# Kernel tuning notes

Measured on AMD Instinct MI355X. Metric: run time of the kernel, lower is better.

The kernel has to match this reference:

```python
import jax, jax.numpy as jnp
import numpy as np

D_MODEL = 512
NH_ATTN = 8
D_STATE = 64
HEADDIM = 128
D_INNER = 2 * D_MODEL          # 1024
NHEADS = D_INNER // HEADDIM    # 8
CONV_K = 4
CONV_DIM = D_INNER + 2 * D_STATE            # 1152
D_IN_PROJ = 2 * D_INNER + 2 * D_STATE + NHEADS  # 2184
B, S, M = 2, 2048, 1024
EPS = 1e-5


def setup_inputs() -> dict:
    key = jax.random.key(0)
    ks = jax.random.split(key, 10)
    s = 0.02
    return {
        'x': jax.random.normal(ks[0], (B, S, D_MODEL), dtype=jnp.float32),
        'memory': jax.random.normal(ks[1], (B, M, D_MODEL), dtype=jnp.float32),
        'pad_mask': jnp.ones((B, S, 1), dtype=jnp.float32),
        'ln1_g': jnp.ones((D_MODEL,)), 'ln1_b': jnp.zeros((D_MODEL,)),
        'ln2_g': jnp.ones((D_MODEL,)), 'ln2_b': jnp.zeros((D_MODEL,)),
        'W_in': jax.random.normal(ks[2], (D_IN_PROJ, D_MODEL)) * s,
        'conv_w': jax.random.normal(ks[3], (CONV_DIM, 1, CONV_K)) * s,
        'conv_b': jnp.zeros((CONV_DIM,)),
        'dt_bias': jnp.log(jnp.expm1(jax.random.uniform(ks[4], (NHEADS,), minval=0.001, maxval=0.1))),
        'A_log': jnp.log(jnp.arange(1, NHEADS + 1, dtype=jnp.float32)),
        'D_skip': jnp.ones((NHEADS,)),
        'rms_w': jnp.ones((D_INNER,)),
        'W_out': jax.random.normal(ks[5], (D_MODEL, D_INNER)) * s,
        'Wqkv': jax.random.normal(ks[6], (3 * D_MODEL, D_MODEL)) * s,
        'bqkv': jnp.zeros((3 * D_MODEL,)),
        'Wo': jax.random.normal(ks[7], (D_MODEL, D_MODEL)) * s,
        'bo': jnp.zeros((D_MODEL,)),
    }


def _layernorm(x, g, b):
    m = jnp.mean(x, axis=-1, keepdims=True)
    v = jnp.mean((x - m) ** 2, axis=-1, keepdims=True)
    return (x - m) * jax.lax.rsqrt(v + EPS) * g + b


def _mamba(x, W_in, conv_w, conv_b, dt_bias, A_log, D_skip, rms_w, W_out):
    b, s, _ = x.shape
    zxbcdt = x @ W_in.T                                     # [b,s,2184]
    z, xBC, dt = jnp.split(zxbcdt, [D_INNER, D_INNER + CONV_DIM], axis=-1)
    # causal depthwise conv over time on (x, B, C)
    xt = jnp.transpose(xBC, (0, 2, 1))                      # [b,C,s]
    xt = jax.lax.conv_general_dilated(
        xt, conv_w, (1,), [(CONV_K - 1, 0)],
        feature_group_count=CONV_DIM,
        dimension_numbers=('NCH', 'OIH', 'NCH'))
    xBC = jax.nn.silu(jnp.transpose(xt, (0, 2, 1)) + conv_b)
    xs, Bm, Cm = jnp.split(xBC, [D_INNER, D_INNER + D_STATE], axis=-1)
    dt = jax.nn.softplus(dt + dt_bias)                      # [b,s,H]
    A = -jnp.exp(A_log)                                     # [H]
    xh = xs.reshape(b, s, NHEADS, HEADDIM)                  # [b,s,H,P]

    def step(h, inps):
        dt_t, B_t, C_t, x_t = inps                          # [b,H],[b,N],[b,N],[b,H,P]
        decay = jnp.exp(dt_t * A)                           # [b,H]
        h = h * decay[..., None, None] + (dt_t[..., None, None] * x_t[..., None]) * B_t[:, None, None, :]
        y = jnp.einsum('bhpn,bn->bhp', h, C_t)
        return h, y

    h0 = jnp.zeros((b, NHEADS, HEADDIM, D_STATE), dtype=x.dtype)
    _, ys = jax.lax.scan(step, h0, (dt.transpose(1, 0, 2), Bm.transpose(1, 0, 2),
                                    Cm.transpose(1, 0, 2), xh.transpose(1, 0, 2, 3)))
    y = ys.transpose(1, 0, 2, 3) + D_skip[None, None, :, None] * xh
    y = y.reshape(b, s, D_INNER) * jax.nn.silu(z)           # gated
    y = y * jax.lax.rsqrt(jnp.mean(y * y, axis=-1, keepdims=True) + EPS) * rms_w
    return y @ W_out.T


def _cross_attn(q_in, memory, Wqkv, bqkv, Wo, bo):
    b, s, _ = q_in.shape
    m = memory.shape[1]
    dh = D_MODEL // NH_ATTN
    q = (q_in @ Wqkv[:D_MODEL].T + bqkv[:D_MODEL]).reshape(b, s, NH_ATTN, dh)
    k = (memory @ Wqkv[D_MODEL:2 * D_MODEL].T + bqkv[D_MODEL:2 * D_MODEL]).reshape(b, m, NH_ATTN, dh)
    v = (memory @ Wqkv[2 * D_MODEL:].T + bqkv[2 * D_MODEL:]).reshape(b, m, NH_ATTN, dh)
    scores = jnp.einsum('bqhd,bkhd->bhqk', q, k) / jnp.sqrt(jnp.asarray(dh, q.dtype))
    p = jax.nn.softmax(scores, axis=-1)
    out = jnp.einsum('bhqk,bkhd->bqhd', p, v).reshape(b, s, D_MODEL)
    return out @ Wo.T + bo


def reference(x, memory, pad_mask, ln1_g, ln1_b, ln2_g, ln2_b, W_in, conv_w, conv_b,
              dt_bias, A_log, D_skip, rms_w, W_out, Wqkv, bqkv, Wo, bo):
    residual = x
    xn = _layernorm(x, ln1_g, ln1_b) * pad_mask
    x = residual + _mamba(xn, W_in, conv_w, conv_b, dt_bias, A_log, D_skip, rms_w, W_out)
    h = _layernorm(x, ln2_g, ln2_b)
    x = x + _cross_attn(h, memory, Wqkv, bqkv, Wo, bo)
    return x
```

## Files before the change

kernel.cpp:

```cpp
#include <hip/hip_runtime.h>
#include <hip/hip_bf16.h>

typedef __hip_bfloat16 bf16;
typedef short v8s __attribute__((ext_vector_type(8)));
typedef float v4f __attribute__((ext_vector_type(4)));

__device__ __forceinline__ void gll16(const bf16* g, bf16* l) {
    __builtin_amdgcn_global_load_lds(
        (const __attribute__((address_space(1))) unsigned int*)g,
        (__attribute__((address_space(3))) unsigned int*)l, 16, 0, 0);
}

__global__ __launch_bounds__(256) void cast_all(
    const float* __restrict__ W_in, const float* __restrict__ W_out,
    const float* __restrict__ Wqkv, const float* __restrict__ Wo,
    const float* __restrict__ mem,
    bf16* __restrict__ Winb, bf16* __restrict__ Woutb, bf16* __restrict__ Wqkvb,
    bf16* __restrict__ Wob, bf16* __restrict__ memb)
{
    int i = blockIdx.x * 256 + threadIdx.x;
    const int E0 = 2184 * 512;
    const int E1 = E0 + 524288;
    const int E2 = E1 + 786432;
    const int E3 = E2 + 262144;
    const int E4 = E3 + 1048576;
    if (i < E0) {
        Winb[i] = __float2bfloat16(W_in[i]);
    } else if (i < E1) {
        int j = i - E0; Woutb[j] = __float2bfloat16(W_out[j]);
    } else if (i < E2) {
        int j = i - E1; Wqkvb[j] = __float2bfloat16(Wqkv[j]);
    } else if (i < E3) {
        int j = i - E2; Wob[j] = __float2bfloat16(Wo[j]);
    } else if (i < E4) {
        int j = i - E3; memb[j] = __float2bfloat16(mem[j]);
    }
}

__global__ __launch_bounds__(256) void ln_kernel(
    const float* __restrict__ x, const float* __restrict__ g,
    const float* __restrict__ bt, const float* __restrict__ mask,
    bf16* __restrict__ out)
{
    int row = blockIdx.x, tid = threadIdx.x;
    const float* xr = x + (size_t)row * 512;
    float v0 = xr[tid], v1 = xr[tid + 256];
    float s = v0 + v1, ss = v0 * v0 + v1 * v1;
    #pragma unroll
    for (int o = 32; o; o >>= 1) { s += __shfl_xor(s, o); ss += __shfl_xor(ss, o); }
    __shared__ float l1[4], l2[4];
    if ((tid & 63) == 0) { l1[tid >> 6] = s; l2[tid >> 6] = ss; }
    __syncthreads();
    s = l1[0] + l1[1] + l1[2] + l1[3];
    ss = l2[0] + l2[1] + l2[2] + l2[3];
    float mean = s * (1.f / 512.f);
    float var = ss * (1.f / 512.f) - mean * mean;
    float rs = rsqrtf(var + 1e-5f);
    float mk = mask ? mask[row] : 1.f;
    out[(size_t)row * 512 + tid] =
        __float2bfloat16(((v0 - mean) * rs * g[tid] + bt[tid]) * mk);
    out[(size_t)row * 512 + tid + 256] =
        __float2bfloat16(((v1 - mean) * rs * g[tid + 256] + bt[tid + 256]) * mk);
}

__global__ __launch_bounds__(256) void gemm_bt(
    const bf16* __restrict__ Aall, const bf16* __restrict__ Wall,
    const float* __restrict__ bias, const float* __restrict__ resid,
    void* __restrict__ Cout,
    int M, int N, int K, int ldA, int ldW, int ldC,
    long sA1, long sA2, long sW1, long sW2, long sC1, long sC2,
    int zdiv, int outbf16)
{
    __shared__ bf16 lA[2][128 * 32];
    __shared__ bf16 lB[2][128 * 32];
    int z = blockIdx.z;
    int zb = z / zdiv, zh = z - zb * zdiv;
    const bf16* A = Aall + zb * sA1 + zh * sA2;
    const bf16* W = Wall + zb * sW1 + zh * sW2;
    long coff = zb * sC1 + zh * sC2;

    int bm = blockIdx.x * 128, bn = blockIdx.y * 128;
    int tid = threadIdx.x, lane = tid & 63, wv = tid >> 6;
    int wr = (wv >> 1) * 64, wc = (wv & 1) * 64;
    int lr15 = lane & 15, lk8 = (lane >> 4) * 8;

    v4f acc[4][4] = {};
    int sr = tid >> 2, sc = (tid & 3) * 8;
    const bf16* Abase = A + (size_t)(bm + sr) * ldA + sc;
    const bf16* Wbase = W + (size_t)(bn + sr) * ldW + sc;

    int nt = K >> 5, cur = 0;
    gll16(Abase, &lA[0][tid * 8]);
    gll16(Abase + (size_t)64 * ldA, &lA[0][tid * 8 + 2048]);
    gll16(Wbase, &lB[0][tid * 8]);
    gll16(Wbase + (size_t)64 * ldW, &lB[0][tid * 8 + 2048]);
    __syncthreads();
    for (int t = 0; t < nt; ++t) {
        if (t + 1 < nt) {
            int k0 = (t + 1) * 32;
            gll16(Abase + k0, &lA[cur ^ 1][tid * 8]);
            gll16(Abase + (size_t)64 * ldA + k0, &lA[cur ^ 1][tid * 8 + 2048]);
            gll16(Wbase + k0, &lB[cur ^ 1][tid * 8]);
            gll16(Wbase + (size_t)64 * ldW + k0, &lB[cur ^ 1][tid * 8 + 2048]);
        }
        v8s af[4], bfr[4];
        #pragma unroll
        for (int i = 0; i < 4; ++i)
            af[i] = *(const v8s*)&lA[cur][(wr + i * 16 + lr15) * 32 + lk8];
        #pragma unroll
        for (int i = 0; i < 4; ++i)
            bfr[i] = *(const v8s*)&lB[cur][(wc + i * 16 + lr15) * 32 + lk8];
        #pragma unroll
        for (int mi = 0; mi < 4; ++mi)
            #pragma unroll
            for (int ni = 0; ni < 4; ++ni)
                acc[mi][ni] = __builtin_amdgcn_mfma_f32_16x16x32_bf16(
                    af[mi], bfr[ni], acc[mi][ni], 0, 0, 0);
        __syncthreads();
        cur ^= 1;
    }
    int r0 = bm + wr + (lane >> 4) * 4;
    int c0 = bn + wc + lr15;
    #pragma unroll
    for (int mi = 0; mi < 4; ++mi) {
        #pragma unroll
        for (int ni = 0; ni < 4; ++ni) {
            int col = c0 + ni * 16;
            if (col < N) {
                float bv = bias ? bias[col] : 0.f;
                #pragma unroll
                for (int r = 0; r < 4; ++r) {
                    int row = r0 + mi * 16 + r;
                    long idx = coff + (long)row * ldC + col;
                    float v = acc[mi][ni][r] + bv;
                    if (resid) v += resid[idx];
                    if (outbf16) ((bf16*)Cout)[idx] = __float2bfloat16(v);
                    else ((float*)Cout)[idx] = v;
                }
            }
        }
    }
}

__global__ __launch_bounds__(256) void gemm64(
    const bf16* __restrict__ Aall, const bf16* __restrict__ Wall,
    const float* __restrict__ bias, const float* __restrict__ resid,
    void* __restrict__ Cout,
    int M, int N, int K, int ldA, int ldW, int ldC,
    long sA1, long sA2, long sW1, long sW2, long sC1, long sC2,
    int zdiv, int outbf16)
{
    __shared__ bf16 lA[2][64 * 32];
    __shared__ bf16 lB[2][64 * 32];
    int z = blockIdx.z;
    int zb = z / zdiv, zh = z - zb * zdiv;
    const bf16* A = Aall + zb * sA1 + zh * sA2;
    const bf16* W = Wall + zb * sW1 + zh * sW2;
    long coff = zb * sC1 + zh * sC2;

    int bm = blockIdx.x * 64, bn = blockIdx.y * 64;
    int tid = threadIdx.x, lane = tid & 63, wv = tid >> 6;
    int wr = (wv >> 1) * 32, wc = (wv & 1) * 32;
    int lr15 = lane & 15, lk8 = (lane >> 4) * 8;

    v4f acc[2][2] = {};
    int sr = tid >> 2, sc = (tid & 3) * 8;
    const bf16* Abase = A + (size_t)(bm + sr) * ldA + sc;
    const bf16* Wbase = W + (size_t)(bn + sr) * ldW + sc;

    int nt = K >> 5, cur = 0;
    gll16(Abase, &lA[0][tid * 8]);
    gll16(Wbase, &lB[0][tid * 8]);
    __syncthreads();
    for (int t = 0; t < nt; ++t) {
        if (t + 1 < nt) {
            int k0 = (t + 1) * 32;
            gll16(Abase + k0, &lA[cur ^ 1][tid * 8]);
            gll16(Wbase + k0, &lB[cur ^ 1][tid * 8]);
        }
        v8s a0 = *(const v8s*)&lA[cur][(wr + lr15) * 32 + lk8];
        v8s a1 = *(const v8s*)&lA[cur][(wr + 16 + lr15) * 32 + lk8];
        v8s b0 = *(const v8s*)&lB[cur][(wc + lr15) * 32 + lk8];
        v8s b1 = *(const v8s*)&lB[cur][(wc + 16 + lr15) * 32 + lk8];
        acc[0][0] = __builtin_amdgcn_mfma_f32_16x16x32_bf16(a0, b0, acc[0][0], 0, 0, 0);
        acc[0][1] = __builtin_amdgcn_mfma_f32_16x16x32_bf16(a0, b1, acc[0][1], 0, 0, 0);
        acc[1][0] = __builtin_amdgcn_mfma_f32_16x16x32_bf16(a1, b0, acc[1][0], 0, 0, 0);
        acc[1][1] = __builtin_amdgcn_mfma_f32_16x16x32_bf16(a1, b1, acc[1][1], 0, 0, 0);
        __syncthreads();
        cur ^= 1;
    }
    int r0 = bm + wr + (lane >> 4) * 4;
    int c0 = bn + wc + lr15;
    #pragma unroll
    for (int mi = 0; mi < 2; ++mi) {
        #pragma unroll
        for (int ni = 0; ni < 2; ++ni) {
            int col = c0 + ni * 16;
            if (col < N) {
                float bv = bias ? bias[col] : 0.f;
                #pragma unroll
                for (int r = 0; r < 4; ++r) {
                    int row = r0 + mi * 16 + r;
                    long idx = coff + (long)row * ldC + col;
                    float v = acc[mi][ni][r] + bv;
                    if (resid) v += resid[idx];
                    if (outbf16) ((bf16*)Cout)[idx] = __float2bfloat16(v);
                    else ((float*)Cout)[idx] = v;
                }
            }
        }
    }
}

__global__ __launch_bounds__(256) void flash_attn(
    const bf16* __restrict__ qb, const bf16* __restrict__ kvb,
    const bf16* __restrict__ vT, bf16* __restrict__ attn)
{
    __shared__ bf16 lK[2][128 * 64];
    __shared__ bf16 lV[2][64 * 128];
    __shared__ bf16 lP[4][16 * 128];
    int z = blockIdx.z;
    int b = z >> 3, h = z & 7;
    int q0 = blockIdx.x * 64;
    int tid = threadIdx.x, lane = tid & 63, wv = tid >> 6;
    int l15 = lane & 15, l4 = lane >> 4, l7 = lane & 7;

    const bf16* Qg = qb + (size_t)(b * 2048 + q0) * 512 + h * 64;
    const bf16* Kg = kvb + (size_t)b * 1024 * 1024 + h * 64;
    const bf16* Vg = vT + (size_t)z * 64 * 1024;

    v8s af[2];
    #pragma unroll
    for (int ks = 0; ks < 2; ++ks)
        af[ks] = *(const v8s*)(Qg + (size_t)(wv * 16 + l15) * 512 + (ks * 4 + l4) * 8);

    #pragma unroll
    for (int pass = 0; pass < 4; ++pass) {
        int s = pass * 256 + tid;
        int kr = s >> 3, kc = s & 7;
        gll16(Kg + (size_t)kr * 1024 + ((kc ^ (kr & 7)) << 3), &lK[0][s * 8]);
        int vr = s >> 4, vc = s & 15;
        int vsw = (vc & 8) | ((vc & 7) ^ (vr & 7));
        gll16(Vg + (size_t)vr * 1024 + (vsw << 3), &lV[0][s * 8]);
    }
    __syncthreads();

    v4f o[4] = {};
    v4f m_run = (v4f){-1e30f, -1e30f, -1e30f, -1e30f};
    v4f l_run = (v4f){0.f, 0.f, 0.f, 0.f};
    bf16* lPw = &lP[wv][0];

    int cur = 0;
    #pragma unroll 1
    for (int t = 0; t < 8; ++t) {
        if (t + 1 < 8) {
            int k0n = (t + 1) * 128;
            #pragma unroll
            for (int pass = 0; pass < 4; ++pass) {
                int s = pass * 256 + tid;
                int kr = s >> 3, kc = s & 7;
                gll16(Kg + (size_t)(k0n + kr) * 1024 + ((kc ^ (kr & 7)) << 3),
                      &lK[cur ^ 1][s * 8]);
                int vr = s >> 4, vc = s & 15;
                int vsw = (vc & 8) | ((vc & 7) ^ (vr & 7));
                gll16(Vg + (size_t)vr * 1024 + k0n + (vsw << 3), &lV[cur ^ 1][s * 8]);
            }
        }
        v4f s_acc[8];
        #pragma unroll
        for (int kn = 0; kn < 8; ++kn) {
            s_acc[kn] = (v4f){0.f, 0.f, 0.f, 0.f};
            #pragma unroll
            for (int ks = 0; ks < 2; ++ks) {
                v8s kv = *(const v8s*)&lK[cur][(kn * 16 + l15) * 64 +
                                               (((ks * 4 + l4) ^ l7) << 3)];
                s_acc[kn] = __builtin_amdgcn_mfma_f32_16x16x32_bf16(
                    af[ks], kv, s_acc[kn], 0, 0, 0);
            }
        }
        v4f tm;
        #pragma unroll
        for (int r = 0; r < 4; ++r) {
            float m0 = fmaxf(fmaxf(s_acc[0][r], s_acc[1][r]),
                             fmaxf(s_acc[2][r], s_acc[3][r]));
            float m1 = fmaxf(fmaxf(s_acc[4][r], s_acc[5][r]),
                             fmaxf(s_acc[6][r], s_acc[7][r]));
            tm[r] = fmaxf(m0, m1);
        }
        #pragma unroll
        for (int off = 8; off >= 1; off >>= 1)
            #pragma unroll
            for (int r = 0; r < 4; ++r)
                tm[r] = fmaxf(tm[r], __shfl_xor(tm[r], off));
        v4f mnew, alpha;
        #pragma unroll
        for (int r = 0; r < 4; ++r) {
            mnew[r] = fmaxf(m_run[r], 0.125f * tm[r]);
            alpha[r] = __expf(m_run[r] - mnew[r]);
        }
        m_run = mnew;
        v4f rs = {0.f, 0.f, 0.f, 0.f};
        #pragma unroll
        for (int kn = 0; kn < 8; ++kn)
            #pragma unroll
            for (int r = 0; r < 4; ++r) {
                float pv = __expf(0.125f * s_acc[kn][r] - mnew[r]);
                s_acc[kn][r] = pv;
                rs[r] += pv;
            }
        #pragma unroll
        for (int off = 8; off >= 1; off >>= 1)
            #pragma unroll
            for (int r = 0; r < 4; ++r)
                rs[r] += __shfl_xor(rs[r], off);
        #pragma unroll
        for (int r = 0; r < 4; ++r)
            l_run[r] = l_run[r] * alpha[r] + rs[r];
        #pragma unroll
        for (int ni = 0; ni < 4; ++ni)
            #pragma unroll
            for (int r = 0; r < 4; ++r)
                o[ni][r] *= alpha[r];
        #pragma unroll
        for (int kn = 0; kn < 8; ++kn)
            #pragma unroll
            for (int r = 0; r < 4; ++r) {
                int row = l4 * 4 + r;
                int col = kn * 16 + l15;
                int c = col >> 3;
                int csw = (c & 8) | ((c & 7) ^ (row & 7));
                lPw[row * 128 + (csw << 3) + (col & 7)] =
                    __float2bfloat16(s_acc[kn][r]);
            }
        #pragma unroll
        for (int ni = 0; ni < 4; ++ni)
            #pragma unroll
            for (int ks = 0; ks < 4; ++ks) {
                int ck = ks * 4 + l4;
                int psw = (ck & 8) | ((ck & 7) ^ l7);
                v8s pv = *(const v8s*)&lPw[l15 * 128 + (psw << 3)];
                v8s vv = *(const v8s*)&lV[cur][(ni * 16 + l15) * 128 + (psw << 3)];
                o[ni] = __builtin_amdgcn_mfma_f32_16x16x32_bf16(
                    pv, vv, o[ni], 0, 0, 0);
            }
        __syncthreads();
        cur ^= 1;
    }
    v4f inv;
    #pragma unroll
    for (int r = 0; r < 4; ++r) inv[r] = 1.f / l_run[r];
    #pragma unroll
    for (int ni = 0; ni < 4; ++ni)
        #pragma unroll
        for (int r = 0; r < 4; ++r) {
            int row = q0 + wv * 16 + l4 * 4 + r;
            int col = h * 64 + ni * 16 + l15;
            attn[(size_t)(b * 2048 + row) * 512 + col] =
                __float2bfloat16(o[ni][r] * inv[r]);
        }
}

__global__ __launch_bounds__(256) void conv_silu(
    const float* __restrict__ zx, const float* __restrict__ cw,
    const float* __restrict__ cb, float* __restrict__ out)
{
    int idx = blockIdx.x * 256 + threadIdx.x;
    if (idx >= 2 * 256 * 288) return;
    int c4 = (idx % 288) * 4;
    int tb = (idx / 288) % 256;
    int b  = idx / (288 * 256);
    int t0 = tb * 8;
    const float* base = zx + (size_t)b * 2048 * 2184 + 1024 + c4;
    float* ob = out + ((size_t)(b * 2048 + t0)) * 1152 + c4;

    float wt[4][4];
    #pragma unroll
    for (int k = 0; k < 4; ++k)
        #pragma unroll
        for (int j = 0; j < 4; ++j) wt[j][k] = cw[(c4 + k) * 4 + j];
    v4f bias = *(const v4f*)(cb + c4);

    v4f r[11];
    #pragma unroll
    for (int j = 0; j < 11; ++j) {
        int ts = t0 - 3 + j;
        if (ts >= 0) r[j] = *(const v4f*)(base + (size_t)ts * 2184);
        else r[j] = (v4f){0.f, 0.f, 0.f, 0.f};
    }
    #pragma unroll
    for (int t = 0; t < 8; ++t) {
        v4f acc = bias;
        #pragma unroll
        for (int k = 0; k < 4; ++k)
            acc[k] += wt[0][k] * r[t][k] + wt[1][k] * r[t + 1][k]
                    + wt[2][k] * r[t + 2][k] + wt[3][k] * r[t + 3][k];
        v4f res;
        #pragma unroll
        for (int k = 0; k < 4; ++k) res[k] = acc[k] / (1.f + expf(-acc[k]));
        *(v4f*)(ob + (size_t)t * 1152) = res;
    }
}

__global__ void dt_prep(const float* __restrict__ zx, const float* __restrict__ dt_bias,
                        const float* __restrict__ A_log,
                        float* __restrict__ dtb, float* __restrict__ decb)
{
    int i = blockIdx.x * 256 + threadIdx.x;
    if (i >= 32768) return;
    int h = i & 7, row = i >> 3;
    float d = zx[(size_t)row * 2184 + 2176 + h] + dt_bias[h];
    float sp = d > 20.f ? d : log1pf(expf(d));
    dtb[i] = sp;
    decb[i] = expf(-expf(A_log[h]) * sp);
}

__global__ __launch_bounds__(256) void scan_p1(
    const float* __restrict__ conv, const float* __restrict__ dtb,
    const float* __restrict__ decb, const float* __restrict__ A_log,
    bf16* __restrict__ slocal, float* __restrict__ cdec)
{
    int chunk = blockIdx.x, bh = blockIdx.y;
    int b = bh >> 3, h = bh & 7;
    int tid = threadIdx.x;
    int wv = tid >> 6, lane = tid & 63;
    int nh = lane >> 5, psub = lane & 31;
    int p = wv * 32 + psub;
    __shared__ float lx[32][128];
    __shared__ float lB[32][64];
    __shared__ float ldt[32], ldec[32];
    const float* cb_ = conv + (size_t)b * 2048 * 1152;
    int t0 = chunk * 32;
    #pragma unroll
    for (int pass = 0; pass < 4; ++pass) {
        int idx = pass * 256 + tid;
        int row = idx >> 5, c4 = (idx & 31) * 4;
        *(v4f*)&lx[row][c4] = *(const v4f*)(cb_ + (size_t)(t0 + row) * 1152 + h * 128 + c4);
    }
    #pragma unroll
    for (int pass = 0; pass < 2; ++pass) {
        int idx = pass * 256 + tid;
        int row = idx >> 4, c4 = (idx & 15) * 4;
        *(v4f*)&lB[row][c4] = *(const v4f*)(cb_ + (size_t)(t0 + row) * 1152 + 1024 + c4);
    }
    if (tid < 32) {
        int ri = (b * 2048 + t0 + tid) * 8 + h;
        ldt[tid] = dtb[ri]; ldec[tid] = decb[ri];
    }
    __syncthreads();
    v4f hs[8] = {};
    float sdt = 0.f;
    #pragma unroll 2
    for (int t = 0; t < 32; ++t) {
        float dtv = ldt[t], dec = ldec[t];
        float c1 = dtv * lx[t][p];
        const v4f* Bp = (const v4f*)&lB[t][nh * 32];
        #pragma unroll
        for (int i = 0; i < 8; ++i) hs[i] = hs[i] * dec + Bp[i] * c1;
        sdt += dtv;
    }
    if (tid == 0) cdec[bh * 64 + chunk] = expf(-expf(A_log[h]) * sdt);
    bf16* S = slocal + ((size_t)bh * 64 + chunk) * 8192;
    #pragma unroll
    for (int i = 0; i < 8; ++i)
        #pragma unroll
        for (int j = 0; j < 4; ++j)
            S[(nh * 32 + i * 4 + j) * 128 + p] = __float2bfloat16(hs[i][j]);
}

__global__ __launch_bounds__(256) void scan_comb(
    const bf16* __restrict__ slocal, const float* __restrict__ cdec,
    bf16* __restrict__ hinit)
{
    int e = blockIdx.x * 256 + threadIdx.x;
    int bh = e >> 13, np = e & 8191;
    size_t base = (size_t)bh * 524288 + np;
    const float* cd = cdec + bh * 64;
    float hi = 0.f;
    for (int c = 0; c < 64; ++c) {
        size_t idx = base + (size_t)c * 8192;
        hinit[idx] = __float2bfloat16(hi);
        hi = hi * cd[c] + __bfloat162float(slocal[idx]);
    }
}

__global__ __launch_bounds__(256) void scan_p3(
    const float* __restrict__ conv, const float* __restrict__ dtb,
    const float* __restrict__ decb, const bf16* __restrict__ hinit,
    const float* __restrict__ Dskip, float* __restrict__ ybuf)
{
    int chunk = blockIdx.x, bh = blockIdx.y;
    int b = bh >> 3, h = bh & 7;
    int tid = threadIdx.x;
    int wv = tid >> 6, lane = tid & 63;
    int nh = lane >> 5, psub = lane & 31;
    int p = wv * 32 + psub;
    __shared__ float lx[32][128];
    __shared__ float lB[32][64];
    __shared__ float lC[32][64];
    __shared__ float ldt[32], ldec[32];
    const float* cb_ = conv + (size_t)b * 2048 * 1152;
    int t0 = chunk * 32;
    #pragma unroll
    for (int pass = 0; pass < 4; ++pass) {
        int idx = pass * 256 + tid;
        int row = idx >> 5, c4 = (idx & 31) * 4;
        *(v4f*)&lx[row][c4] = *(const v4f*)(cb_ + (size_t)(t0 + row) * 1152 + h * 128 + c4);
    }
    #pragma unroll
    for (int pass = 0; pass < 2; ++pass) {
        int idx = pass * 256 + tid;
        int row = idx >> 4, c4 = (idx & 15) * 4;
        *(v4f*)&lB[row][c4] = *(const v4f*)(cb_ + (size_t)(t0 + row) * 1152 + 1024 + c4);
        *(v4f*)&lC[row][c4] = *(const v4f*)(cb_ + (size_t)(t0 + row) * 1152 + 1088 + c4);
    }
    if (tid < 32) {
        int ri = (b * 2048 + t0 + tid) * 8 + h;
        ldt[tid] = dtb[ri]; ldec[tid] = decb[ri];
    }
    __syncthreads();
    v4f hs[8];
    const bf16* H = hinit + ((size_t)bh * 64 + chunk) * 8192;
    #pragma unroll
    for (int i = 0; i < 8; ++i)
        #pragma unroll
        for (int j = 0; j < 4; ++j)
            hs[i][j] = __bfloat162float(H[(nh * 32 + i * 4 + j) * 128 + p]);
    float Dk = Dskip[h];
    #pragma unroll 2
    for (int t = 0; t < 32; ++t) {
        float dtv = ldt[t], dec = ldec[t];
        float xv = lx[t][p];
        float c1 = dtv * xv;
        const v4f* Bp = (const v4f*)&lB[t][nh * 32];
        const v4f* Cp = (const v4f*)&lC[t][nh * 32];
        v4f ya = {0.f, 0.f, 0.f, 0.f};
        #pragma unroll
        for (int i = 0; i < 8; ++i) {
            hs[i] = hs[i] * dec + Bp[i] * c1;
            ya += hs[i] * Cp[i];
        }
        float part = ya[0] + ya[1] + ya[2] + ya[3];
        part += __shfl_xor(part, 32);
        if (nh == 0)
            ybuf[((size_t)(b * 2048 + t0 + t)) * 1024 + h * 128 + p] = part + Dk * xv;
    }
}

__global__ __launch_bounds__(256) void gate_rms(
    const float* __restrict__ ybuf, const float* __restrict__ zx,
    const float* __restrict__ rms_w, bf16* __restrict__ out)
{
    int row = blockIdx.x, tid = threadIdx.x;
    float vals[4];
    float ss = 0.f;
    #pragma unroll
    for (int j = 0; j < 4; ++j) {
        int i = tid + j * 256;
        float y = ybuf[(size_t)row * 1024 + i];
        float zv = zx[(size_t)row * 2184 + i];
        float g = y * (zv / (1.f + expf(-zv)));
        vals[j] = g;
        ss += g * g;
    }
    #pragma unroll
    for (int o = 32; o; o >>= 1) ss += __shfl_xor(ss, o);
    __shared__ float l[4];
    if ((tid & 63) == 0) l[tid >> 6] = ss;
    __syncthreads();
    ss = l[0] + l[1] + l[2] + l[3];
    float rs = rsqrtf(ss * (1.f / 1024.f) + 1e-5f);
    #pragma unroll
    for (int j = 0; j < 4; ++j) {
        int i = tid + j * 256;
        out[(size_t)row * 1024 + i] = __float2bfloat16(vals[j] * rs * rms_w[i]);
    }
}

__global__ __launch_bounds__(256) void v_transpose(const bf16* __restrict__ kvb,
                                                   bf16* __restrict__ vT) {
    __shared__ bf16 t[64][68];
    int bh = blockIdx.y, b = bh >> 3, h = bh & 7;
    int m0 = blockIdx.x * 64;
    int tid = threadIdx.x;
    #pragma unroll
    for (int pass = 0; pass < 2; ++pass) {
        int s = pass * 256 + tid;
        int row = s >> 3, c8 = (s & 7) * 8;
        v8s v = *(const v8s*)(kvb + ((size_t)(b * 1024 + m0 + row)) * 1024 + 512 +
                              h * 64 + c8);
        *(v8s*)&t[row][c8] = v;
    }
    __syncthreads();
    #pragma unroll
    for (int pass = 0; pass < 2; ++pass) {
        int s = pass * 256 + tid;
        int d = s >> 3, m8 = (s & 7) * 8;
        bf16 tmp[8];
        #pragma unroll
        for (int j = 0; j < 8; ++j) tmp[j] = t[m8 + j][d];
        *(v8s*)(vT + ((size_t)(bh * 64 + d)) * 1024 + m0 + m8) = *(v8s*)&tmp[0];
    }
}

extern "C" void kernel_launch(void* const* d_in, const int* in_sizes, int n_in,
                              void* d_out, int out_size, void* d_ws, size_t ws_size,
                              hipStream_t stream) {
    (void)in_sizes; (void)n_in; (void)out_size; (void)ws_size;
    const float* x       = (const float*)d_in[0];
    const float* memory  = (const float*)d_in[1];
    const float* mask    = (const float*)d_in[2];
    const float* ln1_g   = (const float*)d_in[3];
    const float* ln1_b   = (const float*)d_in[4];
    const float* ln2_g   = (const float*)d_in[5];
    const float* ln2_b   = (const float*)d_in[6];
    const float* W_in    = (const float*)d_in[7];
    const float* conv_w  = (const float*)d_in[8];
    const float* conv_b  = (const float*)d_in[9];
    const float* dt_bias = (const float*)d_in[10];
    const float* A_log   = (const float*)d_in[11];
    const float* D_skip  = (const float*)d_in[12];
    const float* rms_w   = (const float*)d_in[13];
    const float* W_out   = (const float*)d_in[14];
    const float* Wqkv    = (const float*)d_in[15];
    const float* bqkv    = (const float*)d_in[16];
    const float* Wo      = (const float*)d_in[17];
    const float* bo      = (const float*)d_in[18];
    float* out = (float*)d_out;

    char* w = (char*)d_ws;
    bf16*  xn     = (bf16*)(w + 0);
    bf16*  Winb   = (bf16*)(w + 4194304);
    bf16*  Woutb  = (bf16*)(w + 6430720);
    bf16*  Wqkvb  = (bf16*)(w + 7479296);
    bf16*  Wob    = (bf16*)(w + 9052160);
    bf16*  memb   = (bf16*)(w + 9576448);
    float* zx     = (float*)(w + 11673600);
    float* conv   = (float*)(w + 47456256);
    float* dtb    = (float*)(w + 66330624);
    float* decb   = (float*)(w + 66461696);
    float* ybuf   = (float*)(w + 66592768);
    bf16*  slocal = (bf16*)(w + 83369984);
    bf16*  hinit  = (bf16*)(w + 100147200);
    bf16*  ybf    = (bf16*)(w + 83369984);
    float* x2     = (float*)(w + 100147200);
    bf16*  hb     = (bf16*)(w + 108535808);
    bf16*  qb     = (bf16*)(w + 112730112);
    float* cdec   = (float*)(w + 116924416);
    bf16*  kvb    = (bf16*)(w + 116928512);
    bf16*  vT     = (bf16*)(w + 121122816);
    bf16*  attn   = (bf16*)(w + 123219968);

    cast_all<<<14608, 256, 0, stream>>>(W_in, W_out, Wqkv, Wo, memory,
                                        Winb, Woutb, Wqkvb, Wob, memb);

    ln_kernel<<<4096, 256, 0, stream>>>(x, ln1_g, ln1_b, mask, xn);

    gemm_bt<<<dim3(32, 18, 1), 256, 0, stream>>>(
        xn, Winb, nullptr, nullptr, (void*)zx,
        4096, 2184, 512, 512, 512, 2184,
        0, 0, 0, 0, 0, 0, 1, 0);

    conv_silu<<<576, 256, 0, stream>>>(zx, conv_w, conv_b, conv);
    dt_prep<<<128, 256, 0, stream>>>(zx, dt_bias, A_log, dtb, decb);

    scan_p1<<<dim3(64, 16), 256, 0, stream>>>(conv, dtb, decb, A_log, slocal, cdec);
    scan_comb<<<512, 256, 0, stream>>>(slocal, cdec, hinit);
    scan_p3<<<dim3(64, 16), 256, 0, stream>>>(conv, dtb, decb, hinit, D_skip, ybuf);

    gate_rms<<<4096, 256, 0, stream>>>(ybuf, zx, rms_w, ybf);

    gemm64<<<dim3(64, 8, 1), 256, 0, stream>>>(
        ybf, Woutb, nullptr, x, (void*)x2,
        4096, 512, 1024, 1024, 1024, 512,
        0, 0, 0, 0, 0, 0, 1, 0);

    ln_kernel<<<4096, 256, 0, stream>>>(x2, ln2_g, ln2_b, nullptr, hb);

    gemm64<<<dim3(64, 8, 1), 256, 0, stream>>>(
        hb, Wqkvb, bqkv, nullptr, (void*)qb,
        4096, 512, 512, 512, 512, 512, 0, 0, 0, 0, 0, 0, 1, 1);
    gemm64<<<dim3(32, 16, 1), 256, 0, stream>>>(
        memb, Wqkvb + 512 * 512, bqkv + 512, nullptr, (void*)kvb,
        2048, 1024, 512, 512, 512, 1024, 0, 0, 0, 0, 0, 0, 1, 1);

    v_transpose<<<dim3(16, 16), 256, 0, stream>>>(kvb, vT);

    flash_attn<<<dim3(32, 1, 16), 256, 0, stream>>>(qb, kvb, vT, attn);

    gemm64<<<dim3(64, 8, 1), 256, 0, stream>>>(
        attn, Wob, bo, x2, (void*)out,
        4096, 512, 512, 512, 512, 512,
        0, 0, 0, 0, 0, 0, 1, 0);
}
```

Before: 208.2 us.

## Store Mamba intermediates in bf16 and fuse small prep kernels

The in_proj GEMM now writes zx in bf16, and the conv output and scan output (ybuf) are also kept in bf16. This roughly halves memory traffic through conv, scan and gate_rms. LayerNorm-1 is merged into the weight-cast kernel, and dt_prep is merged into the conv kernel, which saves two launches. The cost is lower precision in the intermediates, including dt read from bf16, and the gate_rms output buffer is moved to a new workspace offset.

Result: faster. 196.3 us (-5.7%).

```diff
diff --git a/kernel.cpp b/kernel.cpp
--- a/kernel.cpp
+++ b/kernel.cpp
@@ -3,6 +3,7 @@
 
 typedef __hip_bfloat16 bf16;
 typedef short v8s __attribute__((ext_vector_type(8)));
+typedef short v4s __attribute__((ext_vector_type(4)));
 typedef float v4f __attribute__((ext_vector_type(4)));
 
 __device__ __forceinline__ void gll16(const bf16* g, bf16* l) {
@@ -10,15 +11,44 @@
         (const __attribute__((address_space(1))) unsigned int*)g,
         (__attribute__((address_space(3))) unsigned int*)l, 16, 0, 0);
 }
-
-__global__ __launch_bounds__(256) void cast_all(
+__device__ __forceinline__ float bf2f(short s) {
+    return __uint_as_float(((unsigned int)(unsigned short)s) << 16);
+}
+
+__global__ __launch_bounds__(256) void pre_kernel(
+    const float* __restrict__ x, const float* __restrict__ g,
+    const float* __restrict__ bt, const float* __restrict__ mask,
+    bf16* __restrict__ xn,
     const float* __restrict__ W_in, const float* __restrict__ W_out,
     const float* __restrict__ Wqkv, const float* __restrict__ Wo,
     const float* __restrict__ mem,
     bf16* __restrict__ Winb, bf16* __restrict__ Woutb, bf16* __restrict__ Wqkvb,
     bf16* __restrict__ Wob, bf16* __restrict__ memb)
 {
-    int i = blockIdx.x * 256 + threadIdx.x;
+    int tid = threadIdx.x;
+    if (blockIdx.x < 4096) {
+        int row = blockIdx.x;
+        const float* xr = x + (size_t)row * 512;
+        float v0 = xr[tid], v1 = xr[tid + 256];
+        float s = v0 + v1, ss = v0 * v0 + v1 * v1;
+        #pragma unroll
+        for (int o = 32; o; o >>= 1) { s += __shfl_xor(s, o); ss += __shfl_xor(ss, o); }
+        __shared__ float l1[4], l2[4];
+        if ((tid & 63) == 0) { l1[tid >> 6] = s; l2[tid >> 6] = ss; }
+        __syncthreads();
+        s = l1[0] + l1[1] + l1[2] + l1[3];
+        ss = l2[0] + l2[1] + l2[2] + l2[3];
+        float mean = s * (1.f / 512.f);
+        float var = ss * (1.f / 512.f) - mean * mean;
+        float rs = rsqrtf(var + 1e-5f);
+        float mk = mask[row];
+        xn[(size_t)row * 512 + tid] =
+            __float2bfloat16(((v0 - mean) * rs * g[tid] + bt[tid]) * mk);
+        xn[(size_t)row * 512 + tid + 256] =
+            __float2bfloat16(((v1 - mean) * rs * g[tid + 256] + bt[tid + 256]) * mk);
+        return;
+    }
+    int i = (blockIdx.x - 4096) * 256 + tid;
     const int E0 = 2184 * 512;
     const int E1 = E0 + 524288;
     const int E2 = E1 + 786432;
@@ -39,8 +69,7 @@
 
 __global__ __launch_bounds__(256) void ln_kernel(
     const float* __restrict__ x, const float* __restrict__ g,
-    const float* __restrict__ bt, const float* __restrict__ mask,
-    bf16* __restrict__ out)
+    const float* __restrict__ bt, bf16* __restrict__ out)
 {
     int row = blockIdx.x, tid = threadIdx.x;
     const float* xr = x + (size_t)row * 512;
@@ -56,11 +85,10 @@
     float mean = s * (1.f / 512.f);
     float var = ss * (1.f / 512.f) - mean * mean;
     float rs = rsqrtf(var + 1e-5f);
-    float mk = mask ? mask[row] : 1.f;
     out[(size_t)row * 512 + tid] =
-        __float2bfloat16(((v0 - mean) * rs * g[tid] + bt[tid]) * mk);
+        __float2bfloat16((v0 - mean) * rs * g[tid] + bt[tid]);
     out[(size_t)row * 512 + tid + 256] =
-        __float2bfloat16(((v1 - mean) * rs * g[tid + 256] + bt[tid + 256]) * mk);
+        __float2bfloat16((v1 - mean) * rs * g[tid + 256] + bt[tid + 256]);
 }
 
 __global__ __launch_bounds__(256) void gemm_bt(
@@ -360,18 +388,30 @@
         }
 }
 
-__global__ __launch_bounds__(256) void conv_silu(
-    const float* __restrict__ zx, const float* __restrict__ cw,
-    const float* __restrict__ cb, float* __restrict__ out)
-{
-    int idx = blockIdx.x * 256 + threadIdx.x;
-    if (idx >= 2 * 256 * 288) return;
+__global__ __launch_bounds__(256) void conv_dt(
+    const bf16* __restrict__ zx, const float* __restrict__ cw,
+    const float* __restrict__ cb, bf16* __restrict__ out,
+    const float* __restrict__ dt_bias, const float* __restrict__ A_log,
+    float* __restrict__ dtb, float* __restrict__ decb)
+{
+    int tid = threadIdx.x;
+    if (blockIdx.x >= 576) {
+        int i = (blockIdx.x - 576) * 256 + tid;
+        if (i >= 32768) return;
+        int h = i & 7, row = i >> 3;
+        float d = bf2f(((const short*)zx)[(size_t)row * 2184 + 2176 + h]) + dt_bias[h];
+        float sp = d > 20.f ? d : log1pf(expf(d));
+        dtb[i] = sp;
+        decb[i] = expf(-expf(A_log[h]) * sp);
+        return;
+    }
+    int idx = blockIdx.x * 256 + tid;
     int c4 = (idx % 288) * 4;
     int tb = (idx / 288) % 256;
     int b  = idx / (288 * 256);
     int t0 = tb * 8;
-    const float* base = zx + (size_t)b * 2048 * 2184 + 1024 + c4;
-    float* ob = out + ((size_t)(b * 2048 + t0)) * 1152 + c4;
+    const bf16* base = zx + (size_t)b * 2048 * 2184 + 1024 + c4;
+    bf16* ob = out + ((size_t)(b * 2048 + t0)) * 1152 + c4;
 
     float wt[4][4];
     #pragma unroll
@@ -384,8 +424,11 @@
     #pragma unroll
     for (int j = 0; j < 11; ++j) {
         int ts = t0 - 3 + j;
-        if (ts >= 0) r[j] = *(const v4f*)(base + (size_t)ts * 2184);
-        else r[j] = (v4f){0.f, 0.f, 0.f, 0.f};
+        if (ts >= 0) {
+            v4s raw = *(const v4s*)(base + (size_t)ts * 2184);
+            #pragma unroll
+            for (int k = 0; k < 4; ++k) r[j][k] = bf2f(raw[k]);
+        } else r[j] = (v4f){0.f, 0.f, 0.f, 0.f};
     }
     #pragma unroll
     for (int t = 0; t < 8; ++t) {
@@ -394,28 +437,18 @@
         for (int k = 0; k < 4; ++k)
             acc[k] += wt[0][k] * r[t][k] + wt[1][k] * r[t + 1][k]
                     + wt[2][k] * r[t + 2][k] + wt[3][k] * r[t + 3][k];
-        v4f res;
-        #pragma unroll
-        for (int k = 0; k < 4; ++k) res[k] = acc[k] / (1.f + expf(-acc[k]));
-        *(v4f*)(ob + (size_t)t * 1152) = res;
-    }
-}
-
-__global__ void dt_prep(const float* __restrict__ zx, const float* __restrict__ dt_bias,
-                        const float* __restrict__ A_log,
-                        float* __restrict__ dtb, float* __restrict__ decb)
-{
-    int i = blockIdx.x * 256 + threadIdx.x;
-    if (i >= 32768) return;
-    int h = i & 7, row = i >> 3;
-    float d = zx[(size_t)row * 2184 + 2176 + h] + dt_bias[h];
-    float sp = d > 20.f ? d : log1pf(expf(d));
-    dtb[i] = sp;
-    decb[i] = expf(-expf(A_log[h]) * sp);
+        v4s res;
+        #pragma unroll
+        for (int k = 0; k < 4; ++k) {
+            float v = acc[k] / (1.f + expf(-acc[k]));
+            res[k] = (short)__bfloat16_as_ushort(__float2bfloat16(v));
+        }
+        *(v4s*)(ob + (size_t)t * 1152) = res;
+    }
 }
 
 __global__ __launch_bounds__(256) void scan_p1(
-    const float* __restrict__ conv, const float* __restrict__ dtb,
+    const bf16* __restrict__ conv, const float* __restrict__ dtb,
     const float* __restrict__ decb, const float* __restrict__ A_log,
     bf16* __restrict__ slocal, float* __restrict__ cdec)
 {
@@ -428,19 +461,28 @@
     __shared__ float lx[32][128];
     __shared__ float lB[32][64];
     __shared__ float ldt[32], ldec[32];
-    const float* cb_ = conv + (size_t)b * 2048 * 1152;
+    const bf16* cb_ = conv + (size_t)b * 2048 * 1152;
     int t0 = chunk * 32;
     #pragma unroll
-    for (int pass = 0; pass < 4; ++pass) {
-        int idx = pass * 256 + tid;
-        int row = idx >> 5, c4 = (idx & 31) * 4;
-        *(v4f*)&lx[row][c4] = *(const v4f*)(cb_ + (size_t)(t0 + row) * 1152 + h * 128 + c4);
-    }
-    #pragma unroll
     for (int pass = 0; pass < 2; ++pass) {
-        int idx = pass * 256 + tid;
-        int row = idx >> 4, c4 = (idx & 15) * 4;
-        *(v4f*)&lB[row][c4] = *(const v4f*)(cb_ + (size_t)(t0 + row) * 1152 + 1024 + c4);
+        int s = pass * 256 + tid;
+        int row = s >> 4, c8 = (s & 15) * 8;
+        v8s raw = *(const v8s*)(cb_ + (size_t)(t0 + row) * 1152 + h * 128 + c8);
+        v4f lo, hi;
+        #pragma unroll
+        for (int j = 0; j < 4; ++j) { lo[j] = bf2f(raw[j]); hi[j] = bf2f(raw[j + 4]); }
+        *(v4f*)&lx[row][c8] = lo;
+        *(v4f*)&lx[row][c8 + 4] = hi;
+    }
+    {
+        int s = tid;
+        int row = s >> 3, c8 = (s & 7) * 8;
+        v8s raw = *(const v8s*)(cb_ + (size_t)(t0 + row) * 1152 + 1024 + c8);
+        v4f lo, hi;
+        #pragma unroll
+        for (int j = 0; j < 4; ++j) { lo[j] = bf2f(raw[j]); hi[j] = bf2f(raw[j + 4]); }
+        *(v4f*)&lB[row][c8] = lo;
+        *(v4f*)&lB[row][c8 + 4] = hi;
     }
     if (tid < 32) {
         int ri = (b * 2048 + t0 + tid) * 8 + h;
@@ -484,9 +526,9 @@
 }
 
 __global__ __launch_bounds__(256) void scan_p3(
-    const float* __restrict__ conv, const float* __restrict__ dtb,
+    const bf16* __restrict__ conv, const float* __restrict__ dtb,
     const float* __restrict__ decb, const bf16* __restrict__ hinit,
-    const float* __restrict__ Dskip, float* __restrict__ ybuf)
+    const float* __restrict__ Dskip, bf16* __restrict__ ybuf)
 {
     int chunk = blockIdx.x, bh = blockIdx.y;
     int b = bh >> 3, h = bh & 7;
@@ -498,20 +540,33 @@
     __shared__ float lB[32][64];
     __shared__ float lC[32][64];
     __shared__ float ldt[32], ldec[32];
-    const float* cb_ = conv + (size_t)b * 2048 * 1152;
+    const bf16* cb_ = conv + (size_t)b * 2048 * 1152;
     int t0 = chunk * 32;
     #pragma unroll
-    for (int pass = 0; pass < 4; ++pass) {
-        int idx = pass * 256 + tid;
-        int row = idx >> 5, c4 = (idx & 31) * 4;
-        *(v4f*)&lx[row][c4] = *(const v4f*)(cb_ + (size_t)(t0 + row) * 1152 + h * 128 + c4);
-    }
-    #pragma unroll
     for (int pass = 0; pass < 2; ++pass) {
-        int idx = pass * 256 + tid;
-        int row = idx >> 4, c4 = (idx & 15) * 4;
-        *(v4f*)&lB[row][c4] = *(const v4f*)(cb_ + (size_t)(t0 + row) * 1152 + 1024 + c4);
-        *(v4f*)&lC[row][c4] = *(const v4f*)(cb_ + (size_t)(t0 + row) * 1152 + 1088 + c4);
+        int s = pass * 256 + tid;
+        int row = s >> 4, c8 = (s & 15) * 8;
+        v8s raw = *(const v8s*)(cb_ + (size_t)(t0 + row) * 1152 + h * 128 + c8);
+        v4f lo, hi;
+        #pragma unroll
+        for (int j = 0; j < 4; ++j) { lo[j] = bf2f(raw[j]); hi[j] = bf2f(raw[j + 4]); }
+        *(v4f*)&lx[row][c8] = lo;
+        *(v4f*)&lx[row][c8 + 4] = hi;
+    }
+    {
+        int s = tid;
+        int row = s >> 3, c8 = (s & 7) * 8;
+        v8s rawB = *(const v8s*)(cb_ + (size_t)(t0 + row) * 1152 + 1024 + c8);
+        v8s rawC = *(const v8s*)(cb_ + (size_t)(t0 + row) * 1152 + 1088 + c8);
+        v4f lo, hi;
+        #pragma unroll
+        for (int j = 0; j < 4; ++j) { lo[j] = bf2f(rawB[j]); hi[j] = bf2f(rawB[j + 4]); }
+        *(v4f*)&lB[row][c8] = lo;
+        *(v4f*)&lB[row][c8 + 4] = hi;
+        #pragma unroll
+        for (int j = 0; j < 4; ++j) { lo[j] = bf2f(rawC[j]); hi[j] = bf2f(rawC[j + 4]); }
+        *(v4f*)&lC[row][c8] = lo;
+        *(v4f*)&lC[row][c8 + 4] = hi;
     }
     if (tid < 32) {
         int ri = (b * 2048 + t0 + tid) * 8 + h;
@@ -542,23 +597,27 @@
         float part = ya[0] + ya[1] + ya[2] + ya[3];
         part += __shfl_xor(part, 32);
         if (nh == 0)
-            ybuf[((size_t)(b * 2048 + t0 + t)) * 1024 + h * 128 + p] = part + Dk * xv;
+            ybuf[((size_t)(b * 2048 + t0 + t)) * 1024 + h * 128 + p] =
+                __float2bfloat16(part + Dk * xv);
     }
 }
 
 __global__ __launch_bounds__(256) void gate_rms(
-    const float* __restrict__ ybuf, const float* __restrict__ zx,
+    const bf16* __restrict__ ybuf, const bf16* __restrict__ zx,
     const float* __restrict__ rms_w, bf16* __restrict__ out)
 {
     int row = blockIdx.x, tid = threadIdx.x;
+    int i0 = tid * 4;
+    v4s yv = *(const v4s*)(ybuf + (size_t)row * 1024 + i0);
+    v4s zv = *(const v4s*)(zx + (size_t)row * 2184 + i0);
+    v4f rw = *(const v4f*)(rms_w + i0);
     float vals[4];
     float ss = 0.f;
     #pragma unroll
     for (int j = 0; j < 4; ++j) {
-        int i = tid + j * 256;
-        float y = ybuf[(size_t)row * 1024 + i];
-        float zv = zx[(size_t)row * 2184 + i];
-        float g = y * (zv / (1.f + expf(-zv)));
+        float y = bf2f(yv[j]);
+        float z = bf2f(zv[j]);
+        float g = y * (z / (1.f + expf(-z)));
         vals[j] = g;
         ss += g * g;
     }
@@ -569,11 +628,11 @@
     __syncthreads();
     ss = l[0] + l[1] + l[2] + l[3];
     float rs = rsqrtf(ss * (1.f / 1024.f) + 1e-5f);
-    #pragma unroll
-    for (int j = 0; j < 4; ++j) {
-        int i = tid + j * 256;
-        out[(size_t)row * 1024 + i] = __float2bfloat16(vals[j] * rs * rms_w[i]);
-    }
+    v4s o4;
+    #pragma unroll
+    for (int j = 0; j < 4; ++j)
+        o4[j] = (short)__bfloat16_as_ushort(__float2bfloat16(vals[j] * rs * rw[j]));
+    *(v4s*)(out + (size_t)row * 1024 + i0) = o4;
 }
 
 __global__ __launch_bounds__(256) void v_transpose(const bf16* __restrict__ kvb,
@@ -634,11 +693,11 @@
     bf16*  Wqkvb  = (bf16*)(w + 7479296);
     bf16*  Wob    = (bf16*)(w + 9052160);
     bf16*  memb   = (bf16*)(w + 9576448);
-    float* zx     = (float*)(w + 11673600);
-    float* conv   = (float*)(w + 47456256);
+    bf16*  zx     = (bf16*)(w + 11673600);
+    bf16*  conv   = (bf16*)(w + 47456256);
     float* dtb    = (float*)(w + 66330624);
     float* decb   = (float*)(w + 66461696);
-    float* ybuf   = (float*)(w + 66592768);
+    bf16*  ybuf   = (bf16*)(w + 66592768);
     bf16*  slocal = (bf16*)(w + 83369984);
     bf16*  hinit  = (bf16*)(w + 100147200);
     bf16*  ybf    = (bf16*)(w + 83369984);
@@ -649,32 +708,34 @@
     bf16*  kvb    = (bf16*)(w + 116928512);
     bf16*  vT     = (bf16*)(w + 121122816);
     bf16*  attn   = (bf16*)(w + 123219968);
-
-    cast_all<<<14608, 256, 0, stream>>>(W_in, W_out, Wqkv, Wo, memory,
-                                        Winb, Woutb, Wqkvb, Wob, memb);
-
-    ln_kernel<<<4096, 256, 0, stream>>>(x, ln1_g, ln1_b, mask, xn);
+    bf16*  gout   = (bf16*)(w + 75497472);
+    gout = (bf16*)(w + 29564928);
+    (void)ybf;
+
+    pre_kernel<<<18704, 256, 0, stream>>>(x, ln1_g, ln1_b, mask, xn,
+                                          W_in, W_out, Wqkv, Wo, memory,
+                                          Winb, Woutb, Wqkvb, Wob, memb);
 
     gemm_bt<<<dim3(32, 18, 1), 256, 0, stream>>>(
         xn, Winb, nullptr, nullptr, (void*)zx,
         4096, 2184, 512, 512, 512, 2184,
-        0, 0, 0, 0, 0, 0, 1, 0);
-
-    conv_silu<<<576, 256, 0, stream>>>(zx, conv_w, conv_b, conv);
-    dt_prep<<<128, 256, 0, stream>>>(zx, dt_bias, A_log, dtb, decb);
+        0, 0, 0, 0, 0, 0, 1, 1);
+
+    conv_dt<<<704, 256, 0, stream>>>(zx, conv_w, conv_b, conv,
+                                     dt_bias, A_log, dtb, decb);
 
     scan_p1<<<dim3(64, 16), 256, 0, stream>>>(conv, dtb, decb, A_log, slocal, cdec);
     scan_comb<<<512, 256, 0, stream>>>(slocal, cdec, hinit);
     scan_p3<<<dim3(64, 16), 256, 0, stream>>>(conv, dtb, decb, hinit, D_skip, ybuf);
 
-    gate_rms<<<4096, 256, 0, stream>>>(ybuf, zx, rms_w, ybf);
+    gate_rms<<<4096, 256, 0, stream>>>(ybuf, zx, rms_w, gout);
 
     gemm64<<<dim3(64, 8, 1), 256, 0, stream>>>(
-        ybf, Woutb, nullptr, x, (void*)x2,
+        gout, Woutb, nullptr, x, (void*)x2,
         4096, 512, 1024, 1024, 1024, 512,
         0, 0, 0, 0, 0, 0, 1, 0);
 
-    ln_kernel<<<4096, 256, 0, stream>>>(x2, ln2_g, ln2_b, nullptr, hb);
+    ln_kernel<<<4096, 256, 0, stream>>>(x2, ln2_g, ln2_b, hb);
 
     gemm64<<<dim3(64, 8, 1), 256, 0, stream>>>(
         hb, Wqkvb, bqkv, nullptr, (void*)qb,
```
